# Optimization experiments

Hardware: AMD Instinct MI355X
Metric: run time of the kernel (lower is better)

The kernel has to match this reference:

```python
import jax, jax.numpy as jnp
import numpy as np

DIM = 768
NUM_HEADS = 16
HEAD_DIM = DIM // NUM_HEADS
SCALE = HEAD_DIM ** -0.5


def setup_inputs() -> dict:
    key = jax.random.key(0)
    ks = jax.random.split(key, 9)
    B, S = 4, 2048
    init = 1.0 / np.sqrt(DIM)
    x = jax.random.normal(ks[0], (B, S, DIM), dtype=jnp.float32)
    Wq = jax.random.uniform(ks[1], (DIM, DIM), jnp.float32, -init, init)
    bq = jax.random.uniform(ks[2], (DIM,), jnp.float32, -init, init)
    Wk = jax.random.uniform(ks[3], (DIM, DIM), jnp.float32, -init, init)
    bk = jax.random.uniform(ks[4], (DIM,), jnp.float32, -init, init)
    Wv = jax.random.uniform(ks[5], (DIM, DIM), jnp.float32, -init, init)
    bv = jax.random.uniform(ks[6], (DIM,), jnp.float32, -init, init)
    Wo = jax.random.uniform(ks[7], (DIM, DIM), jnp.float32, -init, init)
    bo = jax.random.uniform(ks[8], (DIM,), jnp.float32, -init, init)
    return {"x": x, "Wq": Wq, "bq": bq, "Wk": Wk, "bk": bk,
            "Wv": Wv, "bv": bv, "Wo": Wo, "bo": bo}


def reference(x, Wq, bq, Wk, bk, Wv, bv, Wo, bo):
    B, S, D = x.shape
    H, Hd = NUM_HEADS, HEAD_DIM
    # Linear layers (torch Linear: y = x @ W^T + b); split heads -> [B,H,S,Hd]
    q = (x @ Wq.T + bq).reshape(B, S, H, Hd).transpose(0, 2, 1, 3)
    k = (x @ Wk.T + bk).reshape(B, S, H, Hd).transpose(0, 2, 1, 3)
    v = (x @ Wv.T + bv).reshape(B, S, H, Hd).transpose(0, 2, 1, 3)
    scores = jnp.einsum('bhqd,bhkd->bhqk', q, k) * SCALE  # [B,H,S,S]
    attn = jax.nn.softmax(scores, axis=-1)
    # dropout is identity in eval mode
    out = jnp.einsum('bhqk,bhkd->bhqd', attn, v)
    out = out.transpose(0, 2, 1, 3).reshape(B, S, D)
    return out @ Wo.T + bo
```

## Files before the change

kernel.cpp:

```cpp
#include <hip/hip_runtime.h>

typedef __bf16 bf16_t;
typedef bf16_t bf16x8 __attribute__((ext_vector_type(8)));
typedef _Float16 f16_t;
typedef __fp16 hf16x2 __attribute__((ext_vector_type(2)));
typedef f16_t f16x8 __attribute__((ext_vector_type(8)));
typedef float floatx4 __attribute__((ext_vector_type(4)));
typedef float floatx16 __attribute__((ext_vector_type(16)));

#define S_LEN 2048
#define DIM 768
#define NH 16
#define HD 48
#define HDP 64
#define BHEADS 64
#define ATT_SCALE 0.14433756729740643f
#define W_ELEMS (DIM * DIM)

typedef unsigned short u16;
typedef unsigned int u32;

__device__ __forceinline__ u16 f2b(float f) {
  union { float f; u32 i; } z; z.f = f;
  u32 i = z.i;
  return (u16)((i + 0x7fffu + ((i >> 16) & 1u)) >> 16);
}
__device__ __forceinline__ u32 pack2(float a, float b) {
  return (u32)f2b(a) | ((u32)f2b(b) << 16);
}
__device__ __forceinline__ u32 pkrtz2(float a, float b) {
  union { hf16x2 h; u32 u; } z;
  z.h = __builtin_amdgcn_cvt_pkrtz(a, b);
  return z.u;
}
__device__ __forceinline__ void pl32swap(u32& a, u32& b) {
  asm("v_permlane32_swap_b32 %0, %1" : "+v"(a), "+v"(b));
}

__global__ __launch_bounds__(256) void cvt_all(
    const float* __restrict__ x,
    const float* __restrict__ w0, const float* __restrict__ w1,
    const float* __restrict__ w2, const float* __restrict__ w3,
    u16* __restrict__ x_dst, u16* __restrict__ w_dst)
{
  const int blk = blockIdx.x;
  const float* src;
  u16* dst;
  int idx;
  if (blk < 3072) {
    src = x; dst = x_dst; idx = blk * 256 + threadIdx.x;
  } else {
    int wb = blk - 3072;
    int j = wb / 288;
    src = (j == 0) ? w0 : (j == 1) ? w1 : (j == 2) ? w2 : w3;
    dst = w_dst + (size_t)j * W_ELEMS;
    idx = (wb - j * 288) * 256 + threadIdx.x;
  }
  const float4* s = (const float4*)src;
  float4 a = s[idx * 2], b = s[idx * 2 + 1];
  *(uint4*)&dst[(size_t)idx * 8] =
      make_uint4(pack2(a.x, a.y), pack2(a.z, a.w), pack2(b.x, b.y), pack2(b.z, b.w));
}

__global__ __launch_bounds__(256) void gemm_qkv(
    const u16* __restrict__ A, const u16* __restrict__ Wbase,
    const float* __restrict__ bq, const float* __restrict__ bk,
    const float* __restrict__ bv,
    u16* __restrict__ q_out, u16* __restrict__ k_out, u16* __restrict__ v_out)
{
  __shared__ __attribute__((aligned(16))) u16 smem[8704];
  u16 (*As)[40] = (u16(*)[40])smem;
  u16 (*Bs)[40] = (u16(*)[40])(smem + 5120);

  const int tid = threadIdx.x;
  const int w = tid >> 6, lane = tid & 63, lo = lane & 15, quad = lane >> 4;
  const int bm = blockIdx.x & 63, bn = blockIdx.x >> 6;
  const int mat = bn / 12;
  const int n0 = (bn - mat * 12) * 64;
  const int m0 = bm * 128;
  const u16* W = Wbase + (size_t)mat * W_ELEMS;
  const float* bias = mat == 0 ? bq : (mat == 1 ? bk : bv);
  const float scale = mat == 0 ? ATT_SCALE : 1.0f;

  floatx4 acc[2][4];
#pragma unroll
  for (int mi = 0; mi < 2; mi++)
#pragma unroll
    for (int ni = 0; ni < 4; ni++) acc[mi][ni] = (floatx4){0.f, 0.f, 0.f, 0.f};

  for (int k0 = 0; k0 < DIM; k0 += 32) {
#pragma unroll
    for (int it = 0; it < 2; ++it) {
      int c = tid + it * 256;
      int r = c >> 2, cc = c & 3;
      *(uint4*)&As[r][cc * 8] = *(const uint4*)&A[(size_t)(m0 + r) * DIM + k0 + cc * 8];
    }
    {
      int r = tid >> 2, cc = tid & 3;
      *(uint4*)&Bs[r][cc * 8] = *(const uint4*)&W[(size_t)(n0 + r) * DIM + k0 + cc * 8];
    }
    __syncthreads();
    bf16x8 af[2], bfr[4];
#pragma unroll
    for (int mi = 0; mi < 2; mi++) af[mi] = *(const bf16x8*)&As[w * 32 + mi * 16 + lo][quad * 8];
#pragma unroll
    for (int ni = 0; ni < 4; ni++) bfr[ni] = *(const bf16x8*)&Bs[ni * 16 + lo][quad * 8];
#pragma unroll
    for (int mi = 0; mi < 2; mi++)
#pragma unroll
      for (int ni = 0; ni < 4; ni++)
        acc[mi][ni] = __builtin_amdgcn_mfma_f32_16x16x32_bf16(af[mi], bfr[ni], acc[mi][ni], 0, 0, 0);
    __syncthreads();
  }

  if (mat == 2) {
    u16 (*T)[136] = (u16(*)[136])smem;
#pragma unroll
    for (int mi = 0; mi < 2; mi++)
#pragma unroll
      for (int ni = 0; ni < 4; ni++) {
        int col = ni * 16 + lo;
        float bb = bias[n0 + col];
        float v0 = acc[mi][ni][0] + bb, v1 = acc[mi][ni][1] + bb;
        float v2 = acc[mi][ni][2] + bb, v3 = acc[mi][ni][3] + bb;
        *(uint2*)&T[col][w * 32 + mi * 16 + quad * 4] =
            make_uint2(pkrtz2(v0, v1), pkrtz2(v2, v3));
      }
    __syncthreads();
    const int b = m0 >> 11, s0 = m0 & 2047;
#pragma unroll
    for (int it = 0; it < 4; ++it) {
      int ch = tid + it * 256;
      int col = ch >> 4, sc = ch & 15;
      int gcol = n0 + col;
      int h = gcol / HD, d = gcol - h * HD;
      size_t dst = ((size_t)(b * NH + h) * HDP + d) * S_LEN + s0 + sc * 8;
      *(uint4*)&v_out[dst] = *(const uint4*)&T[col][sc * 8];
    }
    return;
  }

  u16* out = mat == 0 ? q_out : k_out;
#pragma unroll
  for (int mi = 0; mi < 2; mi++)
#pragma unroll
    for (int ni = 0; ni < 4; ni++)
#pragma unroll
      for (int r = 0; r < 4; r++) {
        int row = m0 + w * 32 + mi * 16 + quad * 4 + r;
        int col = n0 + ni * 16 + lo;
        float v = (acc[mi][ni][r] + bias[col]) * scale;
        int b = row >> 11, s = row & 2047;
        int h = col / HD, d = col - h * HD;
        out[((size_t)((b * NH + h) * S_LEN + s)) * HDP + d] = f2b(v);
      }
}

__global__ __launch_bounds__(256) void gemm_wo(
    const u16* __restrict__ A, const u16* __restrict__ W,
    const float* __restrict__ bias, float* __restrict__ out)
{
  __shared__ __attribute__((aligned(16))) u16 smem[8704];
  u16 (*As)[40] = (u16(*)[40])smem;
  u16 (*Bs)[40] = (u16(*)[40])(smem + 5120);

  const int tid = threadIdx.x;
  const int w = tid >> 6, lane = tid & 63, lo = lane & 15, quad = lane >> 4;
  const int bm = blockIdx.x & 63, bn = blockIdx.x >> 6;
  const int m0 = bm * 128, n0 = bn * 64;

  floatx4 acc[2][4];
#pragma unroll
  for (int mi = 0; mi < 2; mi++)
#pragma unroll
    for (int ni = 0; ni < 4; ni++) acc[mi][ni] = (floatx4){0.f, 0.f, 0.f, 0.f};

  for (int k0 = 0; k0 < DIM; k0 += 32) {
#pragma unroll
    for (int it = 0; it < 2; ++it) {
      int c = tid + it * 256;
      int r = c >> 2, cc = c & 3;
      int row = m0 + r, c8 = k0 + cc * 8;
      int h = c8 / HD, d = c8 - h * HD;
      int b = row >> 11, s = row & 2047;
      *(uint4*)&As[r][cc * 8] =
          *(const uint4*)&A[((size_t)((b * NH + h) * S_LEN + s)) * HD + d];
    }
    {
      int r = tid >> 2, cc = tid & 3;
      *(uint4*)&Bs[r][cc * 8] = *(const uint4*)&W[(size_t)(n0 + r) * DIM + k0 + cc * 8];
    }
    __syncthreads();
    bf16x8 af[2], bfr[4];
#pragma unroll
    for (int mi = 0; mi < 2; mi++) af[mi] = *(const bf16x8*)&As[w * 32 + mi * 16 + lo][quad * 8];
#pragma unroll
    for (int ni = 0; ni < 4; ni++) bfr[ni] = *(const bf16x8*)&Bs[ni * 16 + lo][quad * 8];
#pragma unroll
    for (int mi = 0; mi < 2; mi++)
#pragma unroll
      for (int ni = 0; ni < 4; ni++)
        acc[mi][ni] = __builtin_amdgcn_mfma_f32_16x16x32_bf16(af[mi], bfr[ni], acc[mi][ni], 0, 0, 0);
    __syncthreads();
  }

#pragma unroll
  for (int mi = 0; mi < 2; mi++)
#pragma unroll
    for (int ni = 0; ni < 4; ni++)
#pragma unroll
      for (int r = 0; r < 4; r++) {
        int row = m0 + w * 32 + mi * 16 + quad * 4 + r;
        int col = n0 + ni * 16 + lo;
        out[(size_t)row * DIM + col] = acc[mi][ni][r] + bias[col];
      }
}

#define STG_LOAD(k0n) do {                                                     \
  _Pragma("unroll")                                                            \
  for (int it = 0; it < 3; ++it) {                                             \
    int c = tid + it * 256;                                                    \
    if (c < 384) {                                                             \
      int r = c / 6, cc = c - r * 6;                                           \
      stg[it] = *(const uint4*)&K[base + (size_t)((k0n) + r) * HDP + cc * 8];  \
    } else {                                                                   \
      int c2 = c - 384, r = c2 >> 3, cc = c2 & 7;                              \
      stg[it] = *(const uint4*)&V[base + (size_t)r * S_LEN + (k0n) + cc * 8];  \
    }                                                                          \
  }                                                                            \
} while (0)

#define STG_WRITE(bufi) do {                                                   \
  _Pragma("unroll")                                                            \
  for (int it = 0; it < 3; ++it) {                                             \
    int c = tid + it * 256;                                                    \
    if (c < 384) {                                                             \
      int r = c / 6, cc = c - r * 6;                                           \
      *(uint4*)&Ks[bufi][r][cc * 8] = stg[it];                                 \
    } else {                                                                   \
      int c2 = c - 384, r = c2 >> 3, cc = c2 & 7;                              \
      *(uint4*)&Vt[bufi][r][cc * 8] = stg[it];                                 \
    }                                                                          \
  }                                                                            \
} while (0)

__global__ __launch_bounds__(256, 2) void attn_kernel(
    const u16* __restrict__ Q, const u16* __restrict__ K,
    const u16* __restrict__ V, u16* __restrict__ O)
{
  __shared__ __attribute__((aligned(16))) u16 Ks[2][64][56];
  __shared__ __attribute__((aligned(16))) u16 Vt[2][64][72];

  const int tid = threadIdx.x;
  const int w = tid >> 6, lane = tid & 63, l31 = lane & 31, hi = lane >> 5;
  const int flat = blockIdx.x;
  const int xcd = flat & 7, sub = flat >> 3;
  const int bh = xcd * 8 + (sub >> 3);
  const int q0 = (sub & 7) * 256;
  const size_t base = (size_t)bh * S_LEN * HDP;

  bf16x8 qf[2][3];
#pragma unroll
  for (int t = 0; t < 2; t++)
#pragma unroll
    for (int ks = 0; ks < 3; ks++)
      qf[t][ks] = *(const bf16x8*)
          &Q[base + (size_t)(q0 + w * 64 + t * 32 + l31) * HDP + ks * 16 + hi * 8];

  floatx16 oacc[2][2];
#pragma unroll
  for (int t = 0; t < 2; t++)
#pragma unroll
    for (int nd = 0; nd < 2; nd++)
#pragma unroll
      for (int r = 0; r < 16; r++) oacc[t][nd][r] = 0.f;

  float l_lane[2] = {0.f, 0.f};

  uint4 stg[3];
  STG_LOAD(0);
  STG_WRITE(0);

  for (int ti = 0; ti < 32; ++ti) {
    const int cur = ti & 1;
    if (ti < 31) STG_LOAD((ti + 1) * 64);
    __syncthreads();

    bf16x8 ak[2][3];
#pragma unroll
    for (int na = 0; na < 2; na++)
#pragma unroll
      for (int ks = 0; ks < 3; ks++)
        ak[na][ks] = *(const bf16x8*)&Ks[cur][na * 32 + l31][ks * 16 + hi * 8];

    u32 pk[2][2][8];
#pragma unroll
    for (int t = 0; t < 2; t++) {
      floatx16 s0, s1;
#pragma unroll
      for (int r = 0; r < 16; r++) { s0[r] = 0.f; s1[r] = 0.f; }
#pragma unroll
      for (int ks = 0; ks < 3; ks++) {
        s0 = __builtin_amdgcn_mfma_f32_32x32x16_bf16(ak[0][ks], qf[t][ks], s0, 0, 0, 0);
        s1 = __builtin_amdgcn_mfma_f32_32x32x16_bf16(ak[1][ks], qf[t][ks], s1, 0, 0, 0);
      }
#pragma unroll
      for (int m = 0; m < 8; m++) {
        float a0 = __expf(s0[2 * m]), a1 = __expf(s0[2 * m + 1]);
        float b0 = __expf(s1[2 * m]), b1 = __expf(s1[2 * m + 1]);
        l_lane[t] += (a0 + a1) + (b0 + b1);
        pk[t][0][m] = pkrtz2(a0, a1);
        pk[t][1][m] = pkrtz2(b0, b1);
      }
    }

#pragma unroll
    for (int kt = 0; kt < 4; kt++) {
      f16x8 bv0 = *(const f16x8*)&Vt[cur][l31][kt * 16 + hi * 8];
      f16x8 bv1 = *(const f16x8*)&Vt[cur][32 + l31][kt * 16 + hi * 8];
      const int na = kt >> 1, k4 = (kt & 1) * 4;
#pragma unroll
      for (int t = 0; t < 2; t++) {
        u32 w0 = pk[t][na][k4 + 0], w2 = pk[t][na][k4 + 2];
        u32 w1 = pk[t][na][k4 + 1], w3 = pk[t][na][k4 + 3];
        pl32swap(w0, w2);
        pl32swap(w1, w3);
        union { u32 u[4]; f16x8 f; } af;
        af.u[0] = w0; af.u[1] = w1; af.u[2] = w2; af.u[3] = w3;
        oacc[t][0] = __builtin_amdgcn_mfma_f32_32x32x16_f16(af.f, bv0, oacc[t][0], 0, 0, 0);
        oacc[t][1] = __builtin_amdgcn_mfma_f32_32x32x16_f16(af.f, bv1, oacc[t][1], 0, 0, 0);
      }
    }

    if (ti < 31) STG_WRITE(cur ^ 1);
  }

  const size_t obase = (size_t)bh * S_LEN * HD;
  float lt_full[2];
#pragma unroll
  for (int t = 0; t < 2; t++)
    lt_full[t] = l_lane[t] + __shfl_xor(l_lane[t], 32);
#pragma unroll
  for (int t = 0; t < 2; t++) {
#pragma unroll
    for (int r = 0; r < 16; r++) {
      int q_local = (r & 3) + 8 * (r >> 2) + 4 * hi;
      float l_r = __shfl(lt_full[t], q_local);
      float inv = 1.f / l_r;
      int q = q0 + w * 64 + t * 32 + q_local;
      u16* orow = O + obase + (size_t)q * HD;
      orow[l31] = f2b(oacc[t][0][r] * inv);
      if (l31 < 16) orow[32 + l31] = f2b(oacc[t][1][r] * inv);
    }
  }
}

extern "C" void kernel_launch(void* const* d_in, const int* in_sizes, int n_in,
                              void* d_out, int out_size, void* d_ws, size_t ws_size,
                              hipStream_t stream)
{
  const float* x  = (const float*)d_in[0];
  const float* Wq = (const float*)d_in[1];
  const float* bq = (const float*)d_in[2];
  const float* Wk = (const float*)d_in[3];
  const float* bk = (const float*)d_in[4];
  const float* Wv = (const float*)d_in[5];
  const float* bv = (const float*)d_in[6];
  const float* Wo = (const float*)d_in[7];
  const float* bo = (const float*)d_in[8];

  u16* ws   = (u16*)d_ws;
  const size_t qkv_elems = (size_t)BHEADS * S_LEN * HDP;
  u16* q_ws = ws;
  u16* k_ws = q_ws + qkv_elems;
  u16* v_ws = k_ws + qkv_elems;
  u16* x_bf = v_ws + qkv_elems;
  u16* a_ws = x_bf;
  u16* w_bf = x_bf + (size_t)8192 * DIM;
  u16* wo_bf = w_bf + (size_t)3 * W_ELEMS;

  cvt_all<<<dim3(4224), dim3(256), 0, stream>>>(x, Wq, Wk, Wv, Wo, x_bf, w_bf);
  gemm_qkv<<<dim3(2304), dim3(256), 0, stream>>>(x_bf, w_bf, bq, bk, bv,
                                                 q_ws, k_ws, v_ws);
  attn_kernel<<<dim3(512), dim3(256), 0, stream>>>(q_ws, k_ws, v_ws, a_ws);
  gemm_wo<<<dim3(768), dim3(256), 0, stream>>>(a_ws, wo_bf, bo, (float*)d_out);
}
```

Measured before the change: 265.3 us.

## Load GEMM tiles directly into LDS with XOR swizzle and raise MFMA priority

The QKV and output-projection GEMMs now use global_load_lds (direct global-to-LDS DMA) instead of loading through registers. The LDS tiles switch from a padded layout to a dense one with an XOR swizzle so fragment reads avoid bank conflicts. The barrier moves to the top of the loop, and the tile offsets are precomputed once. The attention kernel wraps its MFMA sequences in s_setprio to favour matrix issue over other waves' work. The GEMMs still have a single buffer and two barriers per k-step, so load latency stays exposed, and the swizzled write pattern must match the lane-ordered DMA destinations.

```diff
diff --git a/kernel.cpp b/kernel.cpp
--- a/kernel.cpp
+++ b/kernel.cpp
@@ -35,6 +35,11 @@
 }
 __device__ __forceinline__ void pl32swap(u32& a, u32& b) {
   asm("v_permlane32_swap_b32 %0, %1" : "+v"(a), "+v"(b));
+}
+__device__ __forceinline__ void gld_lds16(const void* g, void* l) {
+  __builtin_amdgcn_global_load_lds(
+      (const __attribute__((address_space(1))) u32*)g,
+      (__attribute__((address_space(3))) u32*)l, 16, 0, 0);
 }
 
 __global__ __launch_bounds__(256) void cvt_all(
@@ -62,6 +67,7 @@
       make_uint4(pack2(a.x, a.y), pack2(a.z, a.w), pack2(b.x, b.y), pack2(b.z, b.w));
 }
 
+
 __global__ __launch_bounds__(256) void gemm_qkv(
     const u16* __restrict__ A, const u16* __restrict__ Wbase,
     const float* __restrict__ bq, const float* __restrict__ bk,
@@ -69,8 +75,8 @@
     u16* __restrict__ q_out, u16* __restrict__ k_out, u16* __restrict__ v_out)
 {
   __shared__ __attribute__((aligned(16))) u16 smem[8704];
-  u16 (*As)[40] = (u16(*)[40])smem;
-  u16 (*Bs)[40] = (u16(*)[40])(smem + 5120);
+  u16* As = smem;
+  u16* Bs = smem + 4096;
 
   const int tid = threadIdx.x;
   const int w = tid >> 6, lane = tid & 63, lo = lane & 15, quad = lane >> 4;
@@ -82,6 +88,20 @@
   const float* bias = mat == 0 ? bq : (mat == 1 ? bk : bv);
   const float scale = mat == 0 ? ATT_SCALE : 1.0f;
 
+  size_t aoff[2];
+#pragma unroll
+  for (int it = 0; it < 2; ++it) {
+    int c = tid + it * 256, r = c >> 2, ccl = c & 3;
+    int ccg = ccl ^ ((r >> 1) & 3);
+    aoff[it] = (size_t)(m0 + r) * DIM + ccg * 8;
+  }
+  size_t boff;
+  {
+    int r = tid >> 2, ccl = tid & 3;
+    int ccg = ccl ^ ((r >> 1) & 3);
+    boff = (size_t)(n0 + r) * DIM + ccg * 8;
+  }
+
   floatx4 acc[2][4];
 #pragma unroll
   for (int mi = 0; mi < 2; mi++)
@@ -89,31 +109,35 @@
     for (int ni = 0; ni < 4; ni++) acc[mi][ni] = (floatx4){0.f, 0.f, 0.f, 0.f};
 
   for (int k0 = 0; k0 < DIM; k0 += 32) {
-#pragma unroll
-    for (int it = 0; it < 2; ++it) {
-      int c = tid + it * 256;
-      int r = c >> 2, cc = c & 3;
-      *(uint4*)&As[r][cc * 8] = *(const uint4*)&A[(size_t)(m0 + r) * DIM + k0 + cc * 8];
-    }
-    {
-      int r = tid >> 2, cc = tid & 3;
-      *(uint4*)&Bs[r][cc * 8] = *(const uint4*)&W[(size_t)(n0 + r) * DIM + k0 + cc * 8];
-    }
-    __syncthreads();
+    __syncthreads();
+#pragma unroll
+    for (int it = 0; it < 2; ++it)
+      gld_lds16(&A[aoff[it] + k0], &As[(it * 256 + w * 64) * 8]);
+    gld_lds16(&W[boff + k0], &Bs[(w * 64) * 8]);
+    __syncthreads();
+
     bf16x8 af[2], bfr[4];
 #pragma unroll
-    for (int mi = 0; mi < 2; mi++) af[mi] = *(const bf16x8*)&As[w * 32 + mi * 16 + lo][quad * 8];
-#pragma unroll
-    for (int ni = 0; ni < 4; ni++) bfr[ni] = *(const bf16x8*)&Bs[ni * 16 + lo][quad * 8];
+    for (int mi = 0; mi < 2; mi++) {
+      int row = w * 32 + mi * 16 + lo;
+      int s = quad ^ ((row >> 1) & 3);
+      af[mi] = *(const bf16x8*)&As[row * 32 + s * 8];
+    }
+#pragma unroll
+    for (int ni = 0; ni < 4; ni++) {
+      int row = ni * 16 + lo;
+      int s = quad ^ ((row >> 1) & 3);
+      bfr[ni] = *(const bf16x8*)&Bs[row * 32 + s * 8];
+    }
 #pragma unroll
     for (int mi = 0; mi < 2; mi++)
 #pragma unroll
       for (int ni = 0; ni < 4; ni++)
         acc[mi][ni] = __builtin_amdgcn_mfma_f32_16x16x32_bf16(af[mi], bfr[ni], acc[mi][ni], 0, 0, 0);
-    __syncthreads();
   }
 
   if (mat == 2) {
+    __syncthreads();
     u16 (*T)[136] = (u16(*)[136])smem;
 #pragma unroll
     for (int mi = 0; mi < 2; mi++)
@@ -160,15 +184,28 @@
     const u16* __restrict__ A, const u16* __restrict__ W,
     const float* __restrict__ bias, float* __restrict__ out)
 {
-  __shared__ __attribute__((aligned(16))) u16 smem[8704];
-  u16 (*As)[40] = (u16(*)[40])smem;
-  u16 (*Bs)[40] = (u16(*)[40])(smem + 5120);
+  __shared__ __attribute__((aligned(16))) u16 smem[6144];
+  u16* As = smem;
+  u16* Bs = smem + 4096;
 
   const int tid = threadIdx.x;
   const int w = tid >> 6, lane = tid & 63, lo = lane & 15, quad = lane >> 4;
   const int bm = blockIdx.x & 63, bn = blockIdx.x >> 6;
   const int m0 = bm * 128, n0 = bn * 64;
 
+  int ar[2], accg[2];
+#pragma unroll
+  for (int it = 0; it < 2; ++it) {
+    int c = tid + it * 256, r = c >> 2, ccl = c & 3;
+    ar[it] = m0 + r;
+    accg[it] = (ccl ^ ((r >> 1) & 3)) * 8;
+  }
+  size_t boff;
+  {
+    int r = tid >> 2, ccl = tid & 3;
+    boff = (size_t)(n0 + r) * DIM + (ccl ^ ((r >> 1) & 3)) * 8;
+  }
+
   floatx4 acc[2][4];
 #pragma unroll
   for (int mi = 0; mi < 2; mi++)
@@ -176,32 +213,36 @@
     for (int ni = 0; ni < 4; ni++) acc[mi][ni] = (floatx4){0.f, 0.f, 0.f, 0.f};
 
   for (int k0 = 0; k0 < DIM; k0 += 32) {
+    __syncthreads();
 #pragma unroll
     for (int it = 0; it < 2; ++it) {
-      int c = tid + it * 256;
-      int r = c >> 2, cc = c & 3;
-      int row = m0 + r, c8 = k0 + cc * 8;
+      int row = ar[it], c8 = k0 + accg[it];
       int h = c8 / HD, d = c8 - h * HD;
       int b = row >> 11, s = row & 2047;
-      *(uint4*)&As[r][cc * 8] =
-          *(const uint4*)&A[((size_t)((b * NH + h) * S_LEN + s)) * HD + d];
-    }
-    {
-      int r = tid >> 2, cc = tid & 3;
-      *(uint4*)&Bs[r][cc * 8] = *(const uint4*)&W[(size_t)(n0 + r) * DIM + k0 + cc * 8];
-    }
-    __syncthreads();
+      gld_lds16(&A[((size_t)((b * NH + h) * S_LEN + s)) * HD + d],
+                &As[(it * 256 + w * 64) * 8]);
+    }
+    gld_lds16(&W[boff + k0], &Bs[(w * 64) * 8]);
+    __syncthreads();
+
     bf16x8 af[2], bfr[4];
 #pragma unroll
-    for (int mi = 0; mi < 2; mi++) af[mi] = *(const bf16x8*)&As[w * 32 + mi * 16 + lo][quad * 8];
-#pragma unroll
-    for (int ni = 0; ni < 4; ni++) bfr[ni] = *(const bf16x8*)&Bs[ni * 16 + lo][quad * 8];
+    for (int mi = 0; mi < 2; mi++) {
+      int row = w * 32 + mi * 16 + lo;
+      int s = quad ^ ((row >> 1) & 3);
+      af[mi] = *(const bf16x8*)&As[row * 32 + s * 8];
+    }
+#pragma unroll
+    for (int ni = 0; ni < 4; ni++) {
+      int row = ni * 16 + lo;
+      int s = quad ^ ((row >> 1) & 3);
+      bfr[ni] = *(const bf16x8*)&Bs[row * 32 + s * 8];
+    }
 #pragma unroll
     for (int mi = 0; mi < 2; mi++)
 #pragma unroll
       for (int ni = 0; ni < 4; ni++)
         acc[mi][ni] = __builtin_amdgcn_mfma_f32_16x16x32_bf16(af[mi], bfr[ni], acc[mi][ni], 0, 0, 0);
-    __syncthreads();
   }
 
 #pragma unroll
@@ -299,11 +340,13 @@
       floatx16 s0, s1;
 #pragma unroll
       for (int r = 0; r < 16; r++) { s0[r] = 0.f; s1[r] = 0.f; }
+      __builtin_amdgcn_s_setprio(1);
 #pragma unroll
       for (int ks = 0; ks < 3; ks++) {
         s0 = __builtin_amdgcn_mfma_f32_32x32x16_bf16(ak[0][ks], qf[t][ks], s0, 0, 0, 0);
         s1 = __builtin_amdgcn_mfma_f32_32x32x16_bf16(ak[1][ks], qf[t][ks], s1, 0, 0, 0);
       }
+      __builtin_amdgcn_s_setprio(0);
 #pragma unroll
       for (int m = 0; m < 8; m++) {
         float a0 = __expf(s0[2 * m]), a1 = __expf(s0[2 * m + 1]);
@@ -327,8 +370,10 @@
         pl32swap(w1, w3);
         union { u32 u[4]; f16x8 f; } af;
         af.u[0] = w0; af.u[1] = w1; af.u[2] = w2; af.u[3] = w3;
+        __builtin_amdgcn_s_setprio(1);
         oacc[t][0] = __builtin_amdgcn_mfma_f32_32x32x16_f16(af.f, bv0, oacc[t][0], 0, 0, 0);
         oacc[t][1] = __builtin_amdgcn_mfma_f32_32x32x16_f16(af.f, bv1, oacc[t][1], 0, 0, 0);
+        __builtin_amdgcn_s_setprio(0);
       }
     }
 
```

Measured after the change: 264.3 us. Within noise of the previous version (-0.4%).
